# Performance work log

Hardware: AMD Instinct MI355X
Metric: run time of the kernel (lower is better)

Reference implementation:

```python
import jax, jax.numpy as jnp
import numpy as np

NUM_HEADS = 8
TOPK = 100


def setup_inputs() -> dict:
    key = jax.random.key(0)
    ks = jax.random.split(key, 8)
    B, N, C = 2, 2048, 512
    q = jax.random.normal(ks[0], (B, N, C), dtype=jnp.float32)
    k = jax.random.normal(ks[1], (B, N, C), dtype=jnp.float32)
    v = jax.random.normal(ks[2], (B, N, C), dtype=jnp.float32)
    w_scale = 0.02
    Wq = jax.random.normal(ks[3], (C, C), dtype=jnp.float32) * w_scale
    Wk = jax.random.normal(ks[4], (C, C), dtype=jnp.float32) * w_scale
    Wv = jax.random.normal(ks[5], (C, C), dtype=jnp.float32) * w_scale
    Wp = jax.random.normal(ks[6], (C, C), dtype=jnp.float32) * w_scale
    bq = jnp.zeros((C,), jnp.float32)
    bk = jnp.zeros((C,), jnp.float32)
    bv = jnp.zeros((C,), jnp.float32)
    bp = jnp.zeros((C,), jnp.float32)
    return {"q": q, "k": k, "v": v, "Wq": Wq, "bq": bq, "Wk": Wk, "bk": bk,
            "Wv": Wv, "bv": bv, "Wp": Wp, "bp": bp}


def reference(q, k, v, Wq, bq, Wk, bk, Wv, bv, Wp, bp):
    B, N, C = q.shape
    H = NUM_HEADS
    D = C // H
    scale = D ** (-0.5)
    # per-head projections: [B, N, C] -> [B, H, N, D]
    qh = (q @ Wq.T + bq).reshape(B, N, H, D).transpose(0, 2, 1, 3)
    kh = (k @ Wk.T + bk).reshape(B, N, H, D).transpose(0, 2, 1, 3)
    vh = (v @ Wv.T + bv).reshape(B, N, H, D).transpose(0, 2, 1, 3)
    # dense scores [B, H, N, N]
    attn = jnp.einsum("bhnd,bhmd->bhnm", qh, kh) * scale
    # top-k mask: equivalent to torch scatter of topk indices (ties are
    # measure-zero for continuous scores). Keep only the topk largest per row.
    top_vals = jax.lax.top_k(attn, TOPK)[0]          # [B, H, N, TOPK]
    thresh = top_vals[..., -1:]                      # k-th largest per row
    attn = jnp.where(attn >= thresh, attn, -jnp.inf)
    attn = jax.nn.softmax(attn, axis=-1)
    out = jnp.einsum("bhnm,bhmd->bhnd", attn, vh)
    out = out.transpose(0, 2, 1, 3).reshape(B, N, C)
    return out @ Wp.T + bp
```

## Files before the change

### kernel.cpp

```cpp
#include <hip/hip_runtime.h>
#include <stdint.h>

#define B_ 2
#define N_ 2048
#define C_ 512
#define H_ 8
#define D_ 64
#define TOPK_ 100
#define BN_ (B_*N_)
#define CAP_ 256

typedef __attribute__((ext_vector_type(8))) short s16x8;
typedef __attribute__((ext_vector_type(8))) unsigned short u16x8;
typedef __attribute__((ext_vector_type(4))) float f32x4;

__device__ __forceinline__ int mbcnt64(unsigned long long m) {
  return __builtin_amdgcn_mbcnt_hi((unsigned)(m >> 32),
         __builtin_amdgcn_mbcnt_lo((unsigned)m, 0u));
}
__device__ __forceinline__ float u2f(unsigned uu) {
  unsigned bits = (uu & 0x80000000u) ? (uu ^ 0x80000000u) : ~uu;
  return __uint_as_float(bits);
}
__device__ __forceinline__ unsigned short bf16rn(float x) {
  unsigned u = __float_as_uint(x);
  unsigned r = (u + 0x7fffu + ((u >> 16) & 1u)) >> 16;
  return (unsigned short)r;
}
__device__ __forceinline__ float bf16f(unsigned short h) {
  return __uint_as_float(((unsigned)h) << 16);
}
__device__ __forceinline__ void split3(float x, unsigned short& h,
                                       unsigned short& m, unsigned short& l) {
  h = bf16rn(x);
  float r1 = x - bf16f(h);
  m = bf16rn(r1);
  float r2 = r1 - bf16f(m);
  l = bf16rn(r2);
}
#define SWZ(r, sl) (((sl) ^ (((r) >> 1) & 3)) << 3)
#define MFMA_BF16(a, b, c) __builtin_amdgcn_mfma_f32_16x16x32_bf16(a, b, c, 0, 0, 0)
#define SIX_PASS(acc, ah, am, al, bh, bm, bl) \
  do { \
    acc = MFMA_BF16(ah, bl, acc); \
    acc = MFMA_BF16(am, bm, acc); \
    acc = MFMA_BF16(al, bh, acc); \
    acc = MFMA_BF16(ah, bm, acc); \
    acc = MFMA_BF16(am, bh, acc); \
    acc = MFMA_BF16(ah, bh, acc); \
  } while (0)

__global__ __launch_bounds__(256)
void wsplit(const float* __restrict__ W0, const float* __restrict__ W1,
            unsigned short* __restrict__ Wsp)
{
  int z = blockIdx.y;
  const float* W = (z == 0) ? W0 : W1;
  const size_t WN = (size_t)C_ * C_;
  unsigned short* Wh = Wsp + (size_t)z * 3 * WN;
  unsigned short* Wm = Wh + WN;
  unsigned short* Wl = Wh + 2 * WN;
  int i = blockIdx.x * 256 + threadIdx.x;
  unsigned short h, m, l;
  split3(W[i], h, m, l);
  Wh[i] = h; Wm[i] = m; Wl[i] = l;
}

__global__ __launch_bounds__(256)
void gemm_qkproj(const float* __restrict__ X0, const float* __restrict__ X1,
                 const float* __restrict__ W0, const float* __restrict__ W1,
                 const float* __restrict__ b0, const float* __restrict__ b1,
                 float* __restrict__ O0, float* __restrict__ O1)
{
  int z = blockIdx.z;
  const float* X = (z == 0) ? X0 : X1;
  const float* W = (z == 0) ? W0 : W1;
  const float* bs = (z == 0) ? b0 : b1;
  float* O = (z == 0) ? O0 : O1;

  __shared__ float Xs[32][128];
  __shared__ float Ws[32][64];

  int t = threadIdx.x;
  int tr = t >> 4, tc = t & 15;
  int m0 = blockIdx.x * 128, c0 = blockIdx.y * 64;

  float acc[8][4] = {};

  for (int k0 = 0; k0 < C_; k0 += 32) {
    #pragma unroll
    for (int j = 0; j < 4; ++j) {
      int fid = t + j * 256;
      int row = fid >> 3;
      int dk  = (fid & 7) << 2;
      int co  = row ^ (dk & 24);
      float4 xv = *(const float4*)(X + (size_t)(m0 + row) * C_ + k0 + dk);
      Xs[dk+0][co] = xv.x; Xs[dk+1][co] = xv.y;
      Xs[dk+2][co] = xv.z; Xs[dk+3][co] = xv.w;
    }
    #pragma unroll
    for (int j = 0; j < 2; ++j) {
      int fid = t + j * 256;
      int cc = fid >> 3;
      int dk = (fid & 7) << 2;
      int co = cc ^ (dk & 24);
      float4 wv = *(const float4*)(W + (size_t)(c0 + cc) * C_ + k0 + dk);
      Ws[dk+0][co] = wv.x; Ws[dk+1][co] = wv.y;
      Ws[dk+2][co] = wv.z; Ws[dk+3][co] = wv.w;
    }
    __syncthreads();
    #pragma unroll
    for (int k = 0; k < 32; ++k) {
      int swz = k & 24;
      float a[8], b[4];
      *(float4*)&a[0] = *(const float4*)&Xs[k][(tr << 3) ^ swz];
      *(float4*)&a[4] = *(const float4*)&Xs[k][((tr << 3) + 4) ^ swz];
      *(float4*)&b[0] = *(const float4*)&Ws[k][(tc << 2) ^ swz];
      #pragma unroll
      for (int i = 0; i < 8; ++i)
        #pragma unroll
        for (int j = 0; j < 4; ++j)
          acc[i][j] = fmaf(a[i], b[j], acc[i][j]);
    }
    __syncthreads();
  }

  float bv[4];
  #pragma unroll
  for (int j = 0; j < 4; ++j) bv[j] = bs[c0 + (tc << 2) + j];

  #pragma unroll
  for (int i = 0; i < 8; ++i) {
    int m = m0 + (tr << 3) + i;
    float4 o = make_float4(acc[i][0] + bv[0], acc[i][1] + bv[1],
                           acc[i][2] + bv[2], acc[i][3] + bv[3]);
    int bb = m >> 11;
    int tok = m & (N_ - 1);
    int h = blockIdx.y;
    *(float4*)(O + (((size_t)(bb * H_ + h) * N_) + tok) * D_ + (tc << 2)) = o;
  }
}

__global__ __launch_bounds__(256)
void gemm_mfma(const float* __restrict__ A,
               const unsigned short* __restrict__ Wplanes,
               const float* __restrict__ bias,
               float* __restrict__ O, int scatter)
{
  const size_t WN = (size_t)C_ * C_;
  const unsigned short* Wh = Wplanes;
  const unsigned short* Wm = Wplanes + WN;
  const unsigned short* Wl = Wplanes + 2 * WN;

  __shared__ unsigned short Ah[128][32], Am[128][32], Al[128][32];
  __shared__ unsigned short Bh[64][32],  Bm[64][32],  Bl[64][32];

  int t = threadIdx.x;
  int l = t & 63, wv = t >> 6;
  int wm = wv >> 1, wn = wv & 1;
  int m0 = blockIdx.x * 128, n0 = blockIdx.y * 64;

  f32x4 acc[4][2];
  #pragma unroll
  for (int i = 0; i < 4; ++i)
    #pragma unroll
    for (int j = 0; j < 2; ++j) acc[i][j] = (f32x4){0.f,0.f,0.f,0.f};

  for (int k0 = 0; k0 < C_; k0 += 32) {
    #pragma unroll
    for (int sj = 0; sj < 2; ++sj) {
      int s = t + sj * 256;
      int r = s >> 2, sl = s & 3, c = sl << 3;
      int co = SWZ(r, sl);
      const float* src = A + (size_t)(m0 + r) * C_ + k0 + c;
      float4 x0 = *(const float4*)src;
      float4 x1 = *(const float4*)(src + 4);
      float xs[8] = {x0.x,x0.y,x0.z,x0.w,x1.x,x1.y,x1.z,x1.w};
      unsigned short hv[8], mv[8], lv[8];
      #pragma unroll
      for (int j = 0; j < 8; ++j) split3(xs[j], hv[j], mv[j], lv[j]);
      *(s16x8*)&Ah[r][co] = *(s16x8*)hv;
      *(s16x8*)&Am[r][co] = *(s16x8*)mv;
      *(s16x8*)&Al[r][co] = *(s16x8*)lv;
    }
    {
      int r = t >> 2, sl = t & 3, c = sl << 3;
      int co = SWZ(r, sl);
      size_t boff = (size_t)(n0 + r) * C_ + k0 + c;
      *(s16x8*)&Bh[r][co] = *(const s16x8*)&Wh[boff];
      *(s16x8*)&Bm[r][co] = *(const s16x8*)&Wm[boff];
      *(s16x8*)&Bl[r][co] = *(const s16x8*)&Wl[boff];
    }
    __syncthreads();

    int lr = l & 15, s0 = l >> 4;
    s16x8 ah[4], am[4], al[4];
    #pragma unroll
    for (int mi = 0; mi < 4; ++mi) {
      int R = wm*64 + mi*16 + lr;
      int co = SWZ(R, s0);
      ah[mi] = *(const s16x8*)&Ah[R][co];
      am[mi] = *(const s16x8*)&Am[R][co];
      al[mi] = *(const s16x8*)&Al[R][co];
    }
    #pragma unroll
    for (int nj = 0; nj < 2; ++nj) {
      int Rb = wn*32 + nj*16 + lr;
      int co = SWZ(Rb, s0);
      s16x8 bh = *(const s16x8*)&Bh[Rb][co];
      s16x8 bm = *(const s16x8*)&Bm[Rb][co];
      s16x8 bl = *(const s16x8*)&Bl[Rb][co];
      #pragma unroll
      for (int mi = 0; mi < 4; ++mi)
        SIX_PASS(acc[mi][nj], ah[mi], am[mi], al[mi], bh, bm, bl);
    }
    __syncthreads();
  }

  int lr = l & 15, lq = l >> 4;
  #pragma unroll
  for (int mi = 0; mi < 4; ++mi) {
    #pragma unroll
    for (int nj = 0; nj < 2; ++nj) {
      #pragma unroll
      for (int r = 0; r < 4; ++r) {
        int m = m0 + wm*64 + mi*16 + lq*4 + r;
        int c = n0 + wn*32 + nj*16 + lr;
        float y = acc[mi][nj][r] + bias[c];
        if (scatter) {
          int bb = m >> 11, tok = m & (N_ - 1);
          int hh = c >> 6, d = c & 63;
          O[(((size_t)(bb * H_ + hh) * N_) + tok) * D_ + d] = y;
        } else {
          O[(size_t)m * C_ + c] = y;
        }
      }
    }
  }
}

__global__ __launch_bounds__(256)
void qk128(const float* __restrict__ qh, const float* __restrict__ kh,
           float* __restrict__ S, int slice0, int row0, int Rrows)
{
  int z = blockIdx.z;
  int slice = slice0 + z;
  const float* Q = qh + (size_t)slice * N_ * D_;
  const float* K = kh + (size_t)slice * N_ * D_;
  float* Sp = S + (size_t)z * Rrows * N_;

  __shared__ float Qs[32][132];
  __shared__ float Ks[32][132];

  int t = threadIdx.x;
  int tr = t >> 4, tc = t & 15;
  int n0 = blockIdx.x * 128, m0 = blockIdx.y * 128;

  float acc[2][2][4][4] = {};

  #pragma unroll
  for (int k0 = 0; k0 < D_; k0 += 32) {
    #pragma unroll
    for (int jj = 0; jj < 4; ++jj) {
      int fid = t + jj * 256;
      int row = fid >> 3;
      int dk  = (fid & 7) << 2;
      float4 qv = *(const float4*)(Q + (size_t)(row0 + n0 + row) * D_ + k0 + dk);
      Qs[dk+0][row] = qv.x; Qs[dk+1][row] = qv.y; Qs[dk+2][row] = qv.z; Qs[dk+3][row] = qv.w;
      float4 kv = *(const float4*)(K + (size_t)(m0 + row) * D_ + k0 + dk);
      Ks[dk+0][row] = kv.x; Ks[dk+1][row] = kv.y; Ks[dk+2][row] = kv.z; Ks[dk+3][row] = kv.w;
    }
    __syncthreads();
    #pragma unroll 8
    for (int k = 0; k < 32; ++k) {
      float a[2][4], b[2][4];
      *(float4*)&a[0][0] = *(const float4*)&Qs[k][tr << 2];
      *(float4*)&a[1][0] = *(const float4*)&Qs[k][64 + (tr << 2)];
      *(float4*)&b[0][0] = *(const float4*)&Ks[k][tc << 2];
      *(float4*)&b[1][0] = *(const float4*)&Ks[k][64 + (tc << 2)];
      #pragma unroll
      for (int ia = 0; ia < 2; ++ia)
        #pragma unroll
        for (int ib = 0; ib < 2; ++ib)
          #pragma unroll
          for (int i = 0; i < 4; ++i)
            #pragma unroll
            for (int j = 0; j < 4; ++j)
              acc[ia][ib][i][j] = fmaf(a[ia][i], b[ib][j], acc[ia][ib][i][j]);
    }
    __syncthreads();
  }

  const float scale = 0.125f;
  #pragma unroll
  for (int ia = 0; ia < 2; ++ia)
    #pragma unroll
    for (int i = 0; i < 4; ++i) {
      int n = n0 + ia*64 + (tr << 2) + i;
      #pragma unroll
      for (int ib = 0; ib < 2; ++ib) {
        float4 o = make_float4(acc[ia][ib][i][0] * scale, acc[ia][ib][i][1] * scale,
                               acc[ia][ib][i][2] * scale, acc[ia][ib][i][3] * scale);
        *(float4*)(Sp + (size_t)n * N_ + m0 + ib*64 + (tc << 2)) = o;
      }
    }
}

__global__ __launch_bounds__(256)
void topk_softmax_pv(const float* __restrict__ S, const float* __restrict__ vh,
                     float* __restrict__ outp, int slice0, int row0, int log2R)
{
  __shared__ float wL[4][CAP_];
  __shared__ unsigned short iL[4][CAP_];

  int t = threadIdx.x;
  int wv = t >> 6;
  int lane = t & 63;
  int gr = blockIdx.x * 4 + wv;
  int s_local = gr >> log2R;
  int rrow = gr & ((1 << log2R) - 1);
  int slice = slice0 + s_local;
  int row = row0 + rrow;

  const float* Srow = S + ((size_t)gr) * N_;

  unsigned u[32];
  #pragma unroll
  for (int i = 0; i < 8; ++i) {
    float4 v = *(const float4*)(Srow + i * 256 + lane * 4);
    float xv[4] = {v.x, v.y, v.z, v.w};
    #pragma unroll
    for (int c = 0; c < 4; ++c) {
      unsigned bits = __float_as_uint(xv[c]);
      u[i*4+c] = bits ^ ((unsigned)(((int)bits) >> 31) | 0x80000000u);
    }
  }

  unsigned mxu = 0u;
  #pragma unroll
  for (int i = 0; i < 32; ++i) mxu = (u[i] > mxu) ? u[i] : mxu;
  #pragma unroll
  for (int off = 32; off >= 1; off >>= 1) {
    unsigned o = (unsigned)__shfl_xor((int)mxu, off);
    mxu = (o > mxu) ? o : mxu;
  }
  unsigned mxs = (unsigned)__builtin_amdgcn_readfirstlane((int)mxu);
  float mx = u2f(mxs);

  unsigned* uList = (unsigned*)&wL[wv][0];
  const float* Vs = vh + (size_t)slice * N_ * D_;

  unsigned thr = 0u;
  int cnt = -1;
  int bitResume = -1;
  for (int bit = 31; bit >= 0; --bit) {
    unsigned cand = thr | (1u << bit);
    if (cand > mxs) continue;
    int c = 0;
    #pragma unroll
    for (int i = 0; i < 32; ++i) c += (u[i] >= cand) ? 1 : 0;
    #pragma unroll
    for (int off = 32; off >= 1; off >>= 1) c += __shfl_xor(c, off);
    if (c >= TOPK_) {
      thr = cand;
      if (c == TOPK_) break;
      if (c <= CAP_) { cnt = c; bitResume = bit - 1; break; }
    }
  }

  float s = 0.f;
  int total = 0;

  if (cnt >= 0) {
    int base = 0;
    #pragma unroll
    for (int i = 0; i < 32; ++i) {
      bool kp = (u[i] >= thr);
      unsigned long long m = __ballot(kp);
      if (kp) {
        int pos = base + mbcnt64(m);
        uList[pos] = u[i];
        iL[wv][pos] = (unsigned short)(((i >> 2) << 8) + (lane << 2) + (i & 3));
      }
      base += __popcll(m);
    }
    for (int bit = bitResume; bit >= 0; --bit) {
      unsigned cand = thr | (1u << bit);
      if (cand > mxs) continue;
      int c = 0;
      for (int e = lane; e < cnt; e += 64) c += (uList[e] >= cand) ? 1 : 0;
      #pragma unroll
      for (int off = 32; off >= 1; off >>= 1) c += __shfl_xor(c, off);
      if (c >= TOPK_) {
        thr = cand;
        if (c == TOPK_) break;
      }
    }
    int base2 = 0;
    for (int e0 = 0; e0 < cnt; e0 += 64) {
      int e = e0 + lane;
      bool valid = (e < cnt);
      unsigned uv = valid ? uList[e] : 0u;
      unsigned short ix = valid ? iL[wv][e] : (unsigned short)0;
      bool kp = valid && (uv >= thr);
      float ev = kp ? __expf(u2f(uv) - mx) : 0.f;
      s += ev;
      unsigned long long m = __ballot(kp);
      if (kp) {
        int pos = base2 + mbcnt64(m);
        wL[wv][pos] = ev;
        iL[wv][pos] = ix;
      }
      base2 += __popcll(m);
    }
    total = base2;
  } else {
    int base = 0;
    #pragma unroll
    for (int i = 0; i < 32; ++i) {
      bool kp = (u[i] >= thr);
      unsigned long long m = __ballot(kp);
      float ev = kp ? __expf(u2f(u[i]) - mx) : 0.f;
      s += ev;
      if (kp) {
        int pos = base + mbcnt64(m);
        if (pos < CAP_) {
          wL[wv][pos] = ev;
          iL[wv][pos] = (unsigned short)(((i >> 2) << 8) + (lane << 2) + (i & 3));
        }
      }
      base += __popcll(m);
    }
    total = base < CAP_ ? base : CAP_;
  }

  #pragma unroll
  for (int off = 32; off >= 1; off >>= 1) s += __shfl_xor(s, off);
  float inv = 1.f / s;

  float a0=0.f,a1=0.f,a2=0.f,a3=0.f,a4=0.f,a5=0.f,a6=0.f,a7=0.f;
  int e = 0;
  for (; e + 8 <= total; e += 8) {
    float4 wa = *(const float4*)&wL[wv][e];
    float4 wb = *(const float4*)&wL[wv][e+4];
    u16x8 jj = *(const u16x8*)&iL[wv][e];
    float v0=Vs[(size_t)jj[0]*D_+lane], v1=Vs[(size_t)jj[1]*D_+lane];
    float v2=Vs[(size_t)jj[2]*D_+lane], v3=Vs[(size_t)jj[3]*D_+lane];
    float v4=Vs[(size_t)jj[4]*D_+lane], v5=Vs[(size_t)jj[5]*D_+lane];
    float v6=Vs[(size_t)jj[6]*D_+lane], v7=Vs[(size_t)jj[7]*D_+lane];
    a0 = fmaf(wa.x, v0, a0); a1 = fmaf(wa.y, v1, a1);
    a2 = fmaf(wa.z, v2, a2); a3 = fmaf(wa.w, v3, a3);
    a4 = fmaf(wb.x, v4, a4); a5 = fmaf(wb.y, v5, a5);
    a6 = fmaf(wb.z, v6, a6); a7 = fmaf(wb.w, v7, a7);
  }
  for (; e < total; ++e)
    a0 = fmaf(wL[wv][e], Vs[(size_t)iL[wv][e] * D_ + lane], a0);
  float acc = (((a0 + a1) + (a2 + a3)) + ((a4 + a5) + (a6 + a7))) * inv;

  int b = slice >> 3;
  int h = slice & 7;
  outp[((size_t)(b * N_ + row)) * C_ + h * D_ + lane] = acc;
}

extern "C" void kernel_launch(void* const* d_in, const int* in_sizes, int n_in,
                              void* d_out, int out_size, void* d_ws, size_t ws_size,
                              hipStream_t stream) {
  const float* q  = (const float*)d_in[0];
  const float* k  = (const float*)d_in[1];
  const float* v  = (const float*)d_in[2];
  const float* Wq = (const float*)d_in[3];
  const float* bq = (const float*)d_in[4];
  const float* Wk = (const float*)d_in[5];
  const float* bk = (const float*)d_in[6];
  const float* Wv = (const float*)d_in[7];
  const float* bv = (const float*)d_in[8];
  const float* Wp = (const float*)d_in[9];
  const float* bp = (const float*)d_in[10];

  const size_t NB = (size_t)B_ * H_ * N_ * D_;
  const size_t WN = (size_t)C_ * C_;
  float* qh  = (float*)d_ws;
  float* kh  = qh + NB;
  float* vh  = kh + NB;
  float* pre = vh + NB;
  unsigned short* Wsp = (unsigned short*)(pre + NB);
  float* S   = (float*)(Wsp + 2 * 3 * WN);

  size_t fixedB = 4 * NB * 4 + 2 * 3 * WN * 2;
  size_t sliceB = (size_t)N_ * N_ * 4;
  size_t avail = (ws_size > fixedB) ? ws_size - fixedB : 0;

  int ns = 1, R = 2048;
  if      (avail >= 16 * sliceB) { ns = 16; R = 2048; }
  else if (avail >= 8 * sliceB)  { ns = 8;  R = 2048; }
  else if (avail >= 4 * sliceB)  { ns = 4;  R = 2048; }
  else if (avail >= 2 * sliceB)  { ns = 2;  R = 2048; }
  else if (avail >= 1 * sliceB)  { ns = 1;  R = 2048; }
  else if (avail >= sliceB / 2)  { ns = 1;  R = 1024; }
  else                           { ns = 1;  R = 512;  }
  int log2R = (R == 2048) ? 11 : ((R == 1024) ? 10 : 9);

  dim3 blk(256);

  wsplit<<<dim3(WN / 256, 2), blk, 0, stream>>>(Wv, Wp, Wsp);

  gemm_qkproj<<<dim3(BN_/128, C_/64, 2), blk, 0, stream>>>(
      q, k, Wq, Wk, bq, bk, qh, kh);

  gemm_mfma<<<dim3(BN_/128, C_/64), blk, 0, stream>>>(
      v, Wsp, bv, vh, 1);

  for (int s0 = 0; s0 < B_ * H_; s0 += ns) {
    int cur = (B_ * H_ - s0) < ns ? (B_ * H_ - s0) : ns;
    for (int r0 = 0; r0 < N_; r0 += R) {
      qk128<<<dim3(R/128, N_/128, cur), blk, 0, stream>>>(qh, kh, S, s0, r0, R);
      topk_softmax_pv<<<dim3(cur * (R/4)), blk, 0, stream>>>(S, vh, pre, s0, r0, log2R);
    }
  }

  gemm_mfma<<<dim3(BN_/128, C_/64), blk, 0, stream>>>(
      pre, Wsp + 3 * WN, bp, (float*)d_out, 0);
}
```

Measured before the change: 361.0 us.

## Shrink Q/K projection tiles to 64x64 and cap attention slice batching at 8

```diff
diff --git a/kernel.cpp b/kernel.cpp
--- a/kernel.cpp
+++ b/kernel.cpp
@@ -67,10 +67,10 @@
 }
 
 __global__ __launch_bounds__(256)
-void gemm_qkproj(const float* __restrict__ X0, const float* __restrict__ X1,
-                 const float* __restrict__ W0, const float* __restrict__ W1,
-                 const float* __restrict__ b0, const float* __restrict__ b1,
-                 float* __restrict__ O0, float* __restrict__ O1)
+void gemm64(const float* __restrict__ X0, const float* __restrict__ X1,
+            const float* __restrict__ W0, const float* __restrict__ W1,
+            const float* __restrict__ b0, const float* __restrict__ b1,
+            float* __restrict__ O0, float* __restrict__ O1)
 {
   int z = blockIdx.z;
   const float* X = (z == 0) ? X0 : X1;
@@ -78,49 +78,38 @@
   const float* bs = (z == 0) ? b0 : b1;
   float* O = (z == 0) ? O0 : O1;
 
-  __shared__ float Xs[32][128];
-  __shared__ float Ws[32][64];
+  __shared__ float Xs[32][68];
+  __shared__ float Ws[32][68];
 
   int t = threadIdx.x;
   int tr = t >> 4, tc = t & 15;
-  int m0 = blockIdx.x * 128, c0 = blockIdx.y * 64;
-
-  float acc[8][4] = {};
+  int m0 = blockIdx.x * 64, c0 = blockIdx.y * 64;
+
+  float acc[4][4] = {};
 
   for (int k0 = 0; k0 < C_; k0 += 32) {
     #pragma unroll
-    for (int j = 0; j < 4; ++j) {
-      int fid = t + j * 256;
+    for (int j2 = 0; j2 < 2; ++j2) {
+      int fid = t + j2 * 256;
       int row = fid >> 3;
       int dk  = (fid & 7) << 2;
-      int co  = row ^ (dk & 24);
       float4 xv = *(const float4*)(X + (size_t)(m0 + row) * C_ + k0 + dk);
-      Xs[dk+0][co] = xv.x; Xs[dk+1][co] = xv.y;
-      Xs[dk+2][co] = xv.z; Xs[dk+3][co] = xv.w;
-    }
-    #pragma unroll
-    for (int j = 0; j < 2; ++j) {
-      int fid = t + j * 256;
-      int cc = fid >> 3;
-      int dk = (fid & 7) << 2;
-      int co = cc ^ (dk & 24);
-      float4 wv = *(const float4*)(W + (size_t)(c0 + cc) * C_ + k0 + dk);
-      Ws[dk+0][co] = wv.x; Ws[dk+1][co] = wv.y;
-      Ws[dk+2][co] = wv.z; Ws[dk+3][co] = wv.w;
+      Xs[dk+0][row] = xv.x; Xs[dk+1][row] = xv.y; Xs[dk+2][row] = xv.z; Xs[dk+3][row] = xv.w;
+      float4 wv = *(const float4*)(W + (size_t)(c0 + row) * C_ + k0 + dk);
+      Ws[dk+0][row] = wv.x; Ws[dk+1][row] = wv.y; Ws[dk+2][row] = wv.z; Ws[dk+3][row] = wv.w;
     }
     __syncthreads();
     #pragma unroll
     for (int k = 0; k < 32; ++k) {
-      int swz = k & 24;
-      float a[8], b[4];
-      *(float4*)&a[0] = *(const float4*)&Xs[k][(tr << 3) ^ swz];
-      *(float4*)&a[4] = *(const float4*)&Xs[k][((tr << 3) + 4) ^ swz];
-      *(float4*)&b[0] = *(const float4*)&Ws[k][(tc << 2) ^ swz];
-      #pragma unroll
-      for (int i = 0; i < 8; ++i)
+      float4 a = *(const float4*)&Xs[k][tr << 2];
+      float4 b = *(const float4*)&Ws[k][tc << 2];
+      float ar[4] = {a.x, a.y, a.z, a.w};
+      float br[4] = {b.x, b.y, b.z, b.w};
+      #pragma unroll
+      for (int i = 0; i < 4; ++i)
         #pragma unroll
         for (int j = 0; j < 4; ++j)
-          acc[i][j] = fmaf(a[i], b[j], acc[i][j]);
+          acc[i][j] = fmaf(ar[i], br[j], acc[i][j]);
     }
     __syncthreads();
   }
@@ -130,10 +119,10 @@
   for (int j = 0; j < 4; ++j) bv[j] = bs[c0 + (tc << 2) + j];
 
   #pragma unroll
-  for (int i = 0; i < 8; ++i) {
-    int m = m0 + (tr << 3) + i;
+  for (int i = 0; i < 4; ++i) {
     float4 o = make_float4(acc[i][0] + bv[0], acc[i][1] + bv[1],
                            acc[i][2] + bv[2], acc[i][3] + bv[3]);
+    int m = m0 + (tr << 2) + i;
     int bb = m >> 11;
     int tok = m & (N_ - 1);
     int h = blockIdx.y;
@@ -491,8 +480,7 @@
   size_t avail = (ws_size > fixedB) ? ws_size - fixedB : 0;
 
   int ns = 1, R = 2048;
-  if      (avail >= 16 * sliceB) { ns = 16; R = 2048; }
-  else if (avail >= 8 * sliceB)  { ns = 8;  R = 2048; }
+  if      (avail >= 8 * sliceB)  { ns = 8;  R = 2048; }
   else if (avail >= 4 * sliceB)  { ns = 4;  R = 2048; }
   else if (avail >= 2 * sliceB)  { ns = 2;  R = 2048; }
   else if (avail >= 1 * sliceB)  { ns = 1;  R = 2048; }
@@ -504,7 +492,7 @@
 
   wsplit<<<dim3(WN / 256, 2), blk, 0, stream>>>(Wv, Wp, Wsp);
 
-  gemm_qkproj<<<dim3(BN_/128, C_/64, 2), blk, 0, stream>>>(
+  gemm64<<<dim3(BN_/64, C_/64, 2), blk, 0, stream>>>(
       q, k, Wq, Wk, bq, bk, qh, kh);
 
   gemm_mfma<<<dim3(BN_/128, C_/64), blk, 0, stream>>>(
```

Measured after the change: 364.8 us. No clear change (+1.1%).
